# Optimization experiments

Hardware: AMD Instinct MI355X
Metric: run time of the kernel (lower is better)

Reference implementation:

```python
import jax, jax.numpy as jnp
import numpy as np

DA = 256      # aux input feature dim
DENSE = 512   # SLAM dense units


def setup_inputs() -> dict:
    key = jax.random.key(0)
    k1, k2, k3, k4 = jax.random.split(key, 4)
    x_main = jax.random.normal(k1, (1, 128, 512, 256), dtype=jnp.float32)  # [1,T,M,K]
    x_aux = jax.random.normal(k2, (256, 128, DA), dtype=jnp.float32)       # [K,T,Da]
    W = jax.random.normal(k3, (DA, DENSE), dtype=jnp.float32) / np.sqrt(DA)
    b = jax.random.normal(k4, (DENSE,), dtype=jnp.float32) * 0.01
    return {"x_main": x_main, "x_aux": x_aux, "W": W, "b": b}


def reference(x_main, x_aux, W, b):
    # SLAM aux dense (+relu), applied to every aux slice at once: [K,T,Da] -> [K,T,dense]
    aux_out = jax.nn.relu(jnp.einsum("ktd,de->kte", x_aux, W) + b)
    main = jnp.squeeze(x_main, axis=0)  # [T,M,K]
    # per-slice matmul main[t] @ aux_out[:,t,:] batched over T
    stacked = jnp.einsum("tmk,kte->tme", main, aux_out)  # [T,M,dense]
    # expand_dims(-1) then expand_dims(0)
    return stacked[None, :, :, :, None]  # [1,T,M,dense,1]
```

## Files before the change

kernel.cpp:

```cpp
#include <hip/hip_runtime.h>


typedef __attribute__((ext_vector_type(8))) short  bf16x8;
typedef __attribute__((ext_vector_type(4))) float  f32x4;
typedef __attribute__((ext_vector_type(4))) unsigned int uint4v;
typedef __attribute__((ext_vector_type(2))) unsigned int uint2v;

#define T_DIM 128
#define M_DIM 512
#define K_DIM 256
#define DA    256
#define DENSE 512
#define AUX_T_STRIDE (K_DIM * DENSE)
#define CHUNK_G_STRIDE (DENSE * 8)

__device__ __forceinline__ unsigned short f2bf(float f) {
    unsigned u = __builtin_bit_cast(unsigned, f);
    unsigned r = (u + 0x7fffu + ((u >> 16) & 1u)) >> 16;
    return (unsigned short)r;
}
__device__ __forceinline__ unsigned pack2(float lo, float hi) {
    return (unsigned)f2bf(lo) | ((unsigned)f2bf(hi) << 16);
}

__global__ __launch_bounds__(256) void wchunk_kernel(const float* __restrict__ W,
                                                     unsigned short* __restrict__ Wc) {
    int c = blockIdx.x * 256 + threadIdx.x;
    int g = c >> 9;
    int e = c & 511;
    float f[8];
#pragma unroll
    for (int j = 0; j < 8; ++j) f[j] = W[(g * 8 + j) * DENSE + e];
    uint4v w;
    w.x = pack2(f[0], f[1]); w.y = pack2(f[2], f[3]);
    w.z = pack2(f[4], f[5]); w.w = pack2(f[6], f[7]);
    *reinterpret_cast<uint4v*>(Wc + (size_t)c * 8) = w;
}

__global__ __launch_bounds__(512) void aux_kernel(const float* __restrict__ xaux,
                                                  const unsigned short* __restrict__ Wc,
                                                  const float* __restrict__ bias,
                                                  unsigned short* __restrict__ auxc) {
    __shared__ unsigned short xa[128][264];
    const int kb = blockIdx.x * 128;
    const int t  = blockIdx.y;
    const int tid = threadIdx.x;
    const int lane = tid & 63, wid = tid >> 6;

    {
        const int d0 = (tid & 63) * 4;
        const int kr = tid >> 6;
#pragma unroll
        for (int p = 0; p < 16; ++p) {
            int k = p * 8 + kr;
            const float* src = xaux + ((size_t)(kb + k) * T_DIM + t) * DA + d0;
            f32x4 v = *reinterpret_cast<const f32x4*>(src);
            uint2v o; o.x = pack2(v.x, v.y); o.y = pack2(v.z, v.w);
            *reinterpret_cast<uint2v*>(&xa[k][d0]) = o;
        }
    }
    __syncthreads();

    const int wk = (wid & 1) * 64;
    const int we = (wid >> 1) * 128;
    const int l15 = lane & 15, lg = lane >> 4;

    f32x4 acc[4][8];
#pragma unroll
    for (int i = 0; i < 4; ++i)
#pragma unroll
        for (int j = 0; j < 8; ++j) acc[i][j] = (f32x4)0.0f;

#define AUX_LOAD_WF(dst, dsv)                                                              \
    do {                                                                                   \
        _Pragma("unroll") for (int j = 0; j < 8; ++j) {                                    \
            int e = we + j * 16 + l15;                                                     \
            dst[j] = *reinterpret_cast<const bf16x8*>(                                     \
                Wc + (size_t)((dsv) * 4 + lg) * CHUNK_G_STRIDE + (size_t)e * 8);           \
        }                                                                                  \
    } while (0)

#define AUX_COMPUTE(wfc, dsv)                                                              \
    do {                                                                                   \
        bf16x8 xf[4];                                                                      \
        _Pragma("unroll") for (int i = 0; i < 4; ++i)                                      \
            xf[i] = *reinterpret_cast<const bf16x8*>(&xa[wk + i * 16 + l15][(dsv) * 32 + lg * 8]); \
        _Pragma("unroll") for (int i = 0; i < 4; ++i)                                      \
            _Pragma("unroll") for (int j = 0; j < 8; ++j)                                  \
                acc[i][j] = __builtin_amdgcn_mfma_f32_16x16x32_bf16(xf[i], wfc[j], acc[i][j], 0, 0, 0); \
    } while (0)

    bf16x8 wfA[8], wfB[8];
    AUX_LOAD_WF(wfA, 0);
#pragma unroll
    for (int ds = 0; ds < 8; ds += 2) {
        AUX_LOAD_WF(wfB, ds + 1);
        AUX_COMPUTE(wfA, ds);
        if (ds + 2 < 8) { AUX_LOAD_WF(wfA, ds + 2); }
        AUX_COMPUTE(wfB, ds + 1);
    }

#pragma unroll
    for (int i = 0; i < 4; ++i) {
        int k0 = kb + wk + i * 16 + lg * 4;
#pragma unroll
        for (int j = 0; j < 8; ++j) {
            int e = we + j * 16 + l15;
            float bv = bias[e];
            float v0 = fmaxf(acc[i][j].x + bv, 0.0f);
            float v1 = fmaxf(acc[i][j].y + bv, 0.0f);
            float v2 = fmaxf(acc[i][j].z + bv, 0.0f);
            float v3 = fmaxf(acc[i][j].w + bv, 0.0f);
            uint2 o; o.x = pack2(v0, v1); o.y = pack2(v2, v3);
            size_t idx = (size_t)t * AUX_T_STRIDE + (size_t)(k0 >> 3) * CHUNK_G_STRIDE
                       + (size_t)e * 8 + (k0 & 7);
            *reinterpret_cast<uint2*>(auxc + idx) = o;
        }
    }
#undef AUX_LOAD_WF
#undef AUX_COMPUTE
}

__global__ __launch_bounds__(256) void main_kernel(const float* __restrict__ xmain,
                                                   const unsigned short* __restrict__ auxc,
                                                   float* __restrict__ out) {
    const int bid = blockIdx.x;
    const int swz = ((bid & 7) << 8) | (bid >> 3);
    const int t   = swz >> 4;
    const int r4  = swz & 15;
    const int eb  = (r4 & 3) * 128;
    const int mb  = (r4 >> 2) * 128;
    const int lane = threadIdx.x & 63, wid = threadIdx.x >> 6;
    const int wm = (wid & 1) * 64;
    const int we = (wid >> 1) * 64;
    const int l15 = lane & 15, lg = lane >> 4;

    const float* At = xmain + (size_t)t * M_DIM * K_DIM;
    const unsigned short* Bt = auxc + (size_t)t * AUX_T_STRIDE;

    f32x4 acc[4][4];
#pragma unroll
    for (int i = 0; i < 4; ++i)
#pragma unroll
        for (int j = 0; j < 4; ++j) acc[i][j] = (f32x4)0.0f;

#define MAIN_LOAD(afd, m0d, m1d, ksv)                                                      \
    do {                                                                                   \
        _Pragma("unroll") for (int i = 0; i < 4; ++i)                                      \
            afd[i] = *reinterpret_cast<const bf16x8*>(                                     \
                Bt + (size_t)((ksv) * 4 + lg) * CHUNK_G_STRIDE                             \
                   + (size_t)(eb + we + i * 16 + l15) * 8);                                \
        _Pragma("unroll") for (int j = 0; j < 4; ++j) {                                    \
            const float* p = At + (size_t)(mb + wm + j * 16 + l15) * K_DIM                 \
                           + (ksv) * 32 + lg * 8;                                          \
            m0d[j] = *reinterpret_cast<const f32x4*>(p);                                   \
            m1d[j] = *reinterpret_cast<const f32x4*>(p + 4);                               \
        }                                                                                  \
    } while (0)

#define MAIN_COMPUTE(afd, m0d, m1d)                                                        \
    do {                                                                                   \
        bf16x8 mf[4];                                                                      \
        _Pragma("unroll") for (int j = 0; j < 4; ++j) {                                    \
            uint4v w;                                                                      \
            w.x = pack2(m0d[j].x, m0d[j].y); w.y = pack2(m0d[j].z, m0d[j].w);              \
            w.z = pack2(m1d[j].x, m1d[j].y); w.w = pack2(m1d[j].z, m1d[j].w);              \
            mf[j] = __builtin_bit_cast(bf16x8, w);                                         \
        }                                                                                  \
        _Pragma("unroll") for (int i = 0; i < 4; ++i)                                      \
            _Pragma("unroll") for (int j = 0; j < 4; ++j)                                  \
                acc[i][j] = __builtin_amdgcn_mfma_f32_16x16x32_bf16(afd[i], mf[j], acc[i][j], 0, 0, 0); \
    } while (0)

    bf16x8 afA[4], afB[4];
    f32x4 m0A[4], m1A[4], m0B[4], m1B[4];
    MAIN_LOAD(afA, m0A, m1A, 0);
#pragma unroll
    for (int ks = 0; ks < 8; ks += 2) {
        MAIN_LOAD(afB, m0B, m1B, ks + 1);
        MAIN_COMPUTE(afA, m0A, m1A);
        if (ks + 2 < 8) { MAIN_LOAD(afA, m0A, m1A, ks + 2); }
        MAIN_COMPUTE(afB, m0B, m1B);
    }
#undef MAIN_LOAD
#undef MAIN_COMPUTE

#pragma unroll
    for (int i = 0; i < 4; ++i) {
        int e0 = eb + we + i * 16 + lg * 4;
#pragma unroll
        for (int j = 0; j < 4; ++j) {
            int m = mb + wm + j * 16 + l15;
            *reinterpret_cast<f32x4*>(out + (size_t)t * M_DIM * DENSE + (size_t)m * DENSE + e0) = acc[i][j];
        }
    }
}

extern "C" void kernel_launch(void* const* d_in, const int* in_sizes, int n_in,
                              void* d_out, int out_size, void* d_ws, size_t ws_size,
                              hipStream_t stream) {
    const float* x_main = (const float*)d_in[0];
    const float* x_aux  = (const float*)d_in[1];
    const float* W      = (const float*)d_in[2];
    const float* b      = (const float*)d_in[3];
    float* out = (float*)d_out;

    unsigned short* Wc   = (unsigned short*)d_ws;
    unsigned short* auxc = (unsigned short*)((char*)d_ws + (1 << 19));

    wchunk_kernel<<<64, 256, 0, stream>>>(W, Wc);
    aux_kernel<<<dim3(2, 128), 512, 0, stream>>>(x_aux, Wc, b, auxc);
    main_kernel<<<2048, 256, 0, stream>>>(x_main, auxc, out);
}
```

Before: 300.2 us.

## Pre-convert x_main to chunked bf16 layout and split aux kernel into more blocks

Adds a kernel that converts x_main to bf16 once, transposing it through LDS into the same k-chunked layout as the aux output. The main GEMM can then load bf16x8 fragments directly instead of reloading and converting fp32 rows for every e-block. The aux kernel is re-tiled from 256 large blocks to 1024 smaller blocks with a swizzled block index to improve occupancy. The cost is an extra launch plus a 32MB intermediate write and read.

```diff
diff --git a/kernel.cpp b/kernel.cpp
--- a/kernel.cpp
+++ b/kernel.cpp
@@ -11,8 +11,8 @@
 #define K_DIM 256
 #define DA    256
 #define DENSE 512
-#define AUX_T_STRIDE (K_DIM * DENSE)
-#define CHUNK_G_STRIDE (DENSE * 8)
+#define CHUNK_T_STRIDE 131072
+#define CHUNK_G_STRIDE 4096
 
 __device__ __forceinline__ unsigned short f2bf(float f) {
     unsigned u = __builtin_bit_cast(unsigned, f);
@@ -37,44 +37,69 @@
     *reinterpret_cast<uint4v*>(Wc + (size_t)c * 8) = w;
 }
 
-__global__ __launch_bounds__(512) void aux_kernel(const float* __restrict__ xaux,
+__global__ __launch_bounds__(256) void xmchunk_kernel(const float* __restrict__ xmain,
+                                                      unsigned short* __restrict__ xmc) {
+    __shared__ unsigned short lds[64 * 256];
+    const int mb = blockIdx.x * 64;
+    const int t  = blockIdx.y;
+    const int tid = threadIdx.x, lane = tid & 63, wid = tid >> 6;
+    char* ldsb = reinterpret_cast<char*>(lds);
+#pragma unroll
+    for (int j = 0; j < 16; ++j) {
+        int mr = wid + 4 * j;
+        const float* src = xmain + ((size_t)(t * M_DIM + mb + mr)) * K_DIM + lane * 4;
+        f32x4 v = *reinterpret_cast<const f32x4*>(src);
+        uint2v o; o.x = pack2(v.x, v.y); o.y = pack2(v.z, v.w);
+        int bofs = mr * 512 + ((lane * 8) ^ ((mr & 7) << 4));
+        *reinterpret_cast<uint2v*>(ldsb + bofs) = o;
+    }
+    __syncthreads();
+#pragma unroll
+    for (int i = 0; i < 8; ++i) {
+        int g = wid * 8 + i;
+        int bofs = lane * 512 + ((g * 16) ^ ((lane & 7) << 4));
+        uint4v c = *reinterpret_cast<const uint4v*>(ldsb + bofs);
+        *reinterpret_cast<uint4v*>(xmc + (size_t)t * CHUNK_T_STRIDE + (size_t)g * CHUNK_G_STRIDE
+                                   + (size_t)(mb + lane) * 8) = c;
+    }
+}
+
+__global__ __launch_bounds__(256) void aux_kernel(const float* __restrict__ xaux,
                                                   const unsigned short* __restrict__ Wc,
                                                   const float* __restrict__ bias,
                                                   unsigned short* __restrict__ auxc) {
-    __shared__ unsigned short xa[128][264];
-    const int kb = blockIdx.x * 128;
-    const int t  = blockIdx.y;
-    const int tid = threadIdx.x;
-    const int lane = tid & 63, wid = tid >> 6;
-
-    {
-        const int d0 = (tid & 63) * 4;
-        const int kr = tid >> 6;
-#pragma unroll
-        for (int p = 0; p < 16; ++p) {
-            int k = p * 8 + kr;
-            const float* src = xaux + ((size_t)(kb + k) * T_DIM + t) * DA + d0;
-            f32x4 v = *reinterpret_cast<const f32x4*>(src);
-            uint2v o; o.x = pack2(v.x, v.y); o.y = pack2(v.z, v.w);
-            *reinterpret_cast<uint2v*>(&xa[k][d0]) = o;
-        }
+    __shared__ unsigned short xa[64 * 264];
+    const int bid = blockIdx.x;
+    const int swz = (bid & 7) * 128 + (bid >> 3);
+    const int t  = swz >> 3;
+    const int r  = swz & 7;
+    const int kb = (r >> 1) * 64;
+    const int eb = (r & 1) * 256;
+    const int tid = threadIdx.x, lane = tid & 63, wid = tid >> 6;
+    const int l15 = lane & 15, lg = lane >> 4;
+    char* xab = reinterpret_cast<char*>(xa);
+
+#pragma unroll
+    for (int j = 0; j < 16; ++j) {
+        int kr = wid + 4 * j;
+        const float* src = xaux + ((size_t)(kb + kr) * T_DIM + t) * DA + lane * 4;
+        f32x4 v = *reinterpret_cast<const f32x4*>(src);
+        uint2v o; o.x = pack2(v.x, v.y); o.y = pack2(v.z, v.w);
+        *reinterpret_cast<uint2v*>(xab + kr * 528 + lane * 8) = o;
     }
     __syncthreads();
 
-    const int wk = (wid & 1) * 64;
-    const int we = (wid >> 1) * 128;
-    const int l15 = lane & 15, lg = lane >> 4;
-
-    f32x4 acc[4][8];
+    const int we = wid * 64;
+    f32x4 acc[4][4];
 #pragma unroll
     for (int i = 0; i < 4; ++i)
 #pragma unroll
-        for (int j = 0; j < 8; ++j) acc[i][j] = (f32x4)0.0f;
+        for (int j = 0; j < 4; ++j) acc[i][j] = (f32x4)0.0f;
 
 #define AUX_LOAD_WF(dst, dsv)                                                              \
     do {                                                                                   \
-        _Pragma("unroll") for (int j = 0; j < 8; ++j) {                                    \
-            int e = we + j * 16 + l15;                                                     \
+        _Pragma("unroll") for (int j = 0; j < 4; ++j) {                                    \
+            int e = eb + we + j * 16 + l15;                                                \
             dst[j] = *reinterpret_cast<const bf16x8*>(                                     \
                 Wc + (size_t)((dsv) * 4 + lg) * CHUNK_G_STRIDE + (size_t)e * 8);           \
         }                                                                                  \
@@ -84,13 +109,14 @@
     do {                                                                                   \
         bf16x8 xf[4];                                                                      \
         _Pragma("unroll") for (int i = 0; i < 4; ++i)                                      \
-            xf[i] = *reinterpret_cast<const bf16x8*>(&xa[wk + i * 16 + l15][(dsv) * 32 + lg * 8]); \
-        _Pragma("unroll") for (int i = 0; i < 4; ++i)                                      \
-            _Pragma("unroll") for (int j = 0; j < 8; ++j)                                  \
+            xf[i] = *reinterpret_cast<const bf16x8*>(                                      \
+                xab + (i * 16 + l15) * 528 + ((dsv) * 4 + lg) * 16);                       \
+        _Pragma("unroll") for (int i = 0; i < 4; ++i)                                      \
+            _Pragma("unroll") for (int j = 0; j < 4; ++j)                                  \
                 acc[i][j] = __builtin_amdgcn_mfma_f32_16x16x32_bf16(xf[i], wfc[j], acc[i][j], 0, 0, 0); \
     } while (0)
 
-    bf16x8 wfA[8], wfB[8];
+    bf16x8 wfA[4], wfB[4];
     AUX_LOAD_WF(wfA, 0);
 #pragma unroll
     for (int ds = 0; ds < 8; ds += 2) {
@@ -99,29 +125,29 @@
         if (ds + 2 < 8) { AUX_LOAD_WF(wfA, ds + 2); }
         AUX_COMPUTE(wfB, ds + 1);
     }
+#undef AUX_LOAD_WF
+#undef AUX_COMPUTE
 
 #pragma unroll
     for (int i = 0; i < 4; ++i) {
-        int k0 = kb + wk + i * 16 + lg * 4;
-#pragma unroll
-        for (int j = 0; j < 8; ++j) {
-            int e = we + j * 16 + l15;
+        int k0 = kb + i * 16 + lg * 4;
+#pragma unroll
+        for (int j = 0; j < 4; ++j) {
+            int e = eb + we + j * 16 + l15;
             float bv = bias[e];
             float v0 = fmaxf(acc[i][j].x + bv, 0.0f);
             float v1 = fmaxf(acc[i][j].y + bv, 0.0f);
             float v2 = fmaxf(acc[i][j].z + bv, 0.0f);
             float v3 = fmaxf(acc[i][j].w + bv, 0.0f);
             uint2 o; o.x = pack2(v0, v1); o.y = pack2(v2, v3);
-            size_t idx = (size_t)t * AUX_T_STRIDE + (size_t)(k0 >> 3) * CHUNK_G_STRIDE
+            size_t idx = (size_t)t * CHUNK_T_STRIDE + (size_t)(k0 >> 3) * CHUNK_G_STRIDE
                        + (size_t)e * 8 + (k0 & 7);
             *reinterpret_cast<uint2*>(auxc + idx) = o;
         }
     }
-#undef AUX_LOAD_WF
-#undef AUX_COMPUTE
-}
-
-__global__ __launch_bounds__(256) void main_kernel(const float* __restrict__ xmain,
+}
+
+__global__ __launch_bounds__(256) void main_kernel(const unsigned short* __restrict__ xmc,
                                                    const unsigned short* __restrict__ auxc,
                                                    float* __restrict__ out) {
     const int bid = blockIdx.x;
@@ -135,8 +161,8 @@
     const int we = (wid >> 1) * 64;
     const int l15 = lane & 15, lg = lane >> 4;
 
-    const float* At = xmain + (size_t)t * M_DIM * K_DIM;
-    const unsigned short* Bt = auxc + (size_t)t * AUX_T_STRIDE;
+    const unsigned short* At = auxc + (size_t)t * CHUNK_T_STRIDE;
+    const unsigned short* Bt = xmc  + (size_t)t * CHUNK_T_STRIDE;
 
     f32x4 acc[4][4];
 #pragma unroll
@@ -144,43 +170,33 @@
 #pragma unroll
         for (int j = 0; j < 4; ++j) acc[i][j] = (f32x4)0.0f;
 
-#define MAIN_LOAD(afd, m0d, m1d, ksv)                                                      \
+#define MAIN_LOAD(afd, mfd, ksv)                                                           \
     do {                                                                                   \
         _Pragma("unroll") for (int i = 0; i < 4; ++i)                                      \
             afd[i] = *reinterpret_cast<const bf16x8*>(                                     \
+                At + (size_t)((ksv) * 4 + lg) * CHUNK_G_STRIDE                             \
+                   + (size_t)(eb + we + i * 16 + l15) * 8);                                \
+        _Pragma("unroll") for (int j = 0; j < 4; ++j)                                      \
+            mfd[j] = *reinterpret_cast<const bf16x8*>(                                     \
                 Bt + (size_t)((ksv) * 4 + lg) * CHUNK_G_STRIDE                             \
-                   + (size_t)(eb + we + i * 16 + l15) * 8);                                \
-        _Pragma("unroll") for (int j = 0; j < 4; ++j) {                                    \
-            const float* p = At + (size_t)(mb + wm + j * 16 + l15) * K_DIM                 \
-                           + (ksv) * 32 + lg * 8;                                          \
-            m0d[j] = *reinterpret_cast<const f32x4*>(p);                                   \
-            m1d[j] = *reinterpret_cast<const f32x4*>(p + 4);                               \
-        }                                                                                  \
-    } while (0)
-
-#define MAIN_COMPUTE(afd, m0d, m1d)                                                        \
-    do {                                                                                   \
-        bf16x8 mf[4];                                                                      \
-        _Pragma("unroll") for (int j = 0; j < 4; ++j) {                                    \
-            uint4v w;                                                                      \
-            w.x = pack2(m0d[j].x, m0d[j].y); w.y = pack2(m0d[j].z, m0d[j].w);              \
-            w.z = pack2(m1d[j].x, m1d[j].y); w.w = pack2(m1d[j].z, m1d[j].w);              \
-            mf[j] = __builtin_bit_cast(bf16x8, w);                                         \
-        }                                                                                  \
+                   + (size_t)(mb + wm + j * 16 + l15) * 8);                                \
+    } while (0)
+
+#define MAIN_COMPUTE(afd, mfd)                                                             \
+    do {                                                                                   \
         _Pragma("unroll") for (int i = 0; i < 4; ++i)                                      \
             _Pragma("unroll") for (int j = 0; j < 4; ++j)                                  \
-                acc[i][j] = __builtin_amdgcn_mfma_f32_16x16x32_bf16(afd[i], mf[j], acc[i][j], 0, 0, 0); \
-    } while (0)
-
-    bf16x8 afA[4], afB[4];
-    f32x4 m0A[4], m1A[4], m0B[4], m1B[4];
-    MAIN_LOAD(afA, m0A, m1A, 0);
+                acc[i][j] = __builtin_amdgcn_mfma_f32_16x16x32_bf16(afd[i], mfd[j], acc[i][j], 0, 0, 0); \
+    } while (0)
+
+    bf16x8 afA[4], afB[4], mfA[4], mfB[4];
+    MAIN_LOAD(afA, mfA, 0);
 #pragma unroll
     for (int ks = 0; ks < 8; ks += 2) {
-        MAIN_LOAD(afB, m0B, m1B, ks + 1);
-        MAIN_COMPUTE(afA, m0A, m1A);
-        if (ks + 2 < 8) { MAIN_LOAD(afA, m0A, m1A, ks + 2); }
-        MAIN_COMPUTE(afB, m0B, m1B);
+        MAIN_LOAD(afB, mfB, ks + 1);
+        MAIN_COMPUTE(afA, mfA);
+        if (ks + 2 < 8) { MAIN_LOAD(afA, mfA, ks + 2); }
+        MAIN_COMPUTE(afB, mfB);
     }
 #undef MAIN_LOAD
 #undef MAIN_COMPUTE
@@ -206,9 +222,11 @@
     float* out = (float*)d_out;
 
     unsigned short* Wc   = (unsigned short*)d_ws;
-    unsigned short* auxc = (unsigned short*)((char*)d_ws + (1 << 19));
+    unsigned short* auxc = (unsigned short*)((char*)d_ws + (1u << 19));
+    unsigned short* xmc  = (unsigned short*)((char*)d_ws + (1u << 19) + (1u << 25));
 
     wchunk_kernel<<<64, 256, 0, stream>>>(W, Wc);
-    aux_kernel<<<dim3(2, 128), 512, 0, stream>>>(x_aux, Wc, b, auxc);
-    main_kernel<<<2048, 256, 0, stream>>>(x_main, auxc, out);
-}
+    xmchunk_kernel<<<dim3(8, 128), 256, 0, stream>>>(x_main, xmc);
+    aux_kernel<<<1024, 256, 0, stream>>>(x_aux, Wc, b, auxc);
+    main_kernel<<<2048, 256, 0, stream>>>(xmc, auxc, out);
+}
```

Result: faster. 257.1 us (-14.4%).
